# Kernel tuning notes

Hardware: AMD Instinct MI355X
Metric: run time of the kernel (lower is better)

## Reference

```python
import jax, jax.numpy as jnp
import numpy as np

DIM = 1024
NUM_HEADS = 16
HEAD_DIM = DIM // NUM_HEADS
EPS = 1e-5


def setup_inputs() -> dict:
    key = jax.random.key(0)
    ks = jax.random.split(key, 8)
    B, N = 4, 2048
    s = 0.02
    return {
        "x1": jax.random.normal(ks[0], (B, N, DIM), jnp.float32),
        "x2": jax.random.normal(ks[1], (B, N, DIM), jnp.float32),
        "wq": jax.random.normal(ks[2], (DIM, DIM), jnp.float32) * s,
        "bq": jnp.zeros((DIM,), jnp.float32),
        "wkv": jax.random.normal(ks[3], (DIM, 2 * DIM), jnp.float32) * s,
        "bkv": jnp.zeros((2 * DIM,), jnp.float32),
        "gamma_q": jnp.ones((HEAD_DIM,), jnp.float32),
        "beta_q": jnp.zeros((HEAD_DIM,), jnp.float32),
        "gamma_k": jnp.ones((HEAD_DIM,), jnp.float32),
        "beta_k": jnp.zeros((HEAD_DIM,), jnp.float32),
    }


def _layernorm(x, gamma, beta):
    m = jnp.mean(x, axis=-1, keepdims=True)
    v = jnp.mean(jnp.square(x - m), axis=-1, keepdims=True)
    return (x - m) * jax.lax.rsqrt(v + EPS) * gamma + beta


def reference(x1, x2, wq, bq, wkv, bkv, gamma_q, beta_q, gamma_k, beta_k):
    B, N, C = x1.shape
    H, D = NUM_HEADS, C // NUM_HEADS
    q = x1 @ wq + bq                      # [B,N,C]
    kv = x2 @ wkv + bkv                   # [B,N,2C]
    k, v = kv[..., :C], kv[..., C:]
    # [B,N,C] -> [B,H,N,D]
    q = q.reshape(B, N, H, D).transpose(0, 2, 1, 3)
    k = k.reshape(B, N, H, D).transpose(0, 2, 1, 3)
    v = v.reshape(B, N, H, D).transpose(0, 2, 1, 3)
    q = _layernorm(q, gamma_q, beta_q)
    k = _layernorm(k, gamma_k, beta_k)
    scale = 1.0 / jnp.sqrt(jnp.asarray(D, x1.dtype))
    scores = jnp.einsum("bhnd,bhmd->bhnm", q, k) * scale
    attn = jax.nn.softmax(scores, axis=-1)
    out = jnp.einsum("bhnm,bhmd->bhnd", attn, v)  # [B,H,N,D]
    return out.transpose(0, 2, 1, 3).reshape(B, N, C)
```

## Files before the change

### kernel.cpp

```cpp
#include <hip/hip_runtime.h>
#include <hip/hip_bf16.h>

#define NHEADS 16
#define HDIM 64
#define BATCH 4
#define SEQ 2048
#define CDIM 1024
#define ROWS (BATCH * SEQ)
#define QSCALE (0.125f * 1.44269504088896f)

typedef __attribute__((ext_vector_type(8))) short short8;
typedef __attribute__((ext_vector_type(4))) float f32x4;
typedef __attribute__((ext_vector_type(4))) unsigned int u32x4;
typedef __attribute__((ext_vector_type(2))) unsigned int u32x2;

__device__ inline short f2bf(float f) {
    unsigned int u = __builtin_bit_cast(unsigned int, f);
    unsigned int r = (u + 0x7fffu + ((u >> 16) & 1u)) >> 16;
    return (short)r;
}

__device__ __forceinline__ void gll16(const void* g, void* l) {
    __builtin_amdgcn_global_load_lds(
        (const __attribute__((address_space(1))) unsigned int*)g,
        (__attribute__((address_space(3))) unsigned int*)l, 16, 0, 0);
}

__device__ __forceinline__ unsigned int pack_bf2(float a, float b) {
    return __builtin_amdgcn_perm(__builtin_bit_cast(unsigned int, b),
                                 __builtin_bit_cast(unsigned int, a), 0x07060302u);
}

__global__ __launch_bounds__(256) void cvt_bf16(const float* __restrict__ src,
                                                short* __restrict__ dst, int n8) {
    int i = blockIdx.x * 256 + threadIdx.x;
    if (i < n8) {
        f32x4 a = ((const f32x4*)src)[i * 2];
        f32x4 b = ((const f32x4*)src)[i * 2 + 1];
        short8 o;
        o[0] = f2bf(a[0]); o[1] = f2bf(a[1]); o[2] = f2bf(a[2]); o[3] = f2bf(a[3]);
        o[4] = f2bf(b[0]); o[5] = f2bf(b[1]); o[6] = f2bf(b[2]); o[7] = f2bf(b[3]);
        ((short8*)dst)[i] = o;
    }
}

__global__ __launch_bounds__(256) void wtrans(const float* __restrict__ W,
                                              short* __restrict__ WT, int Nw) {
    __shared__ short T[64][72];
    const int t = threadIdx.x;
    const int n0 = blockIdx.x * 64, k0 = blockIdx.y * 64;
    const int kl = t >> 2, c4 = (t & 3) * 16;
    const float* src = W + (size_t)(k0 + kl) * Nw + n0 + c4;
    short8 s0, s1;
#pragma unroll
    for (int e = 0; e < 2; e++) {
        f32x4 u = *(const f32x4*)(src + e * 4);
        s0[e * 4 + 0] = f2bf(u[0]); s0[e * 4 + 1] = f2bf(u[1]);
        s0[e * 4 + 2] = f2bf(u[2]); s0[e * 4 + 3] = f2bf(u[3]);
        f32x4 v = *(const f32x4*)(src + 8 + e * 4);
        s1[e * 4 + 0] = f2bf(v[0]); s1[e * 4 + 1] = f2bf(v[1]);
        s1[e * 4 + 2] = f2bf(v[2]); s1[e * 4 + 3] = f2bf(v[3]);
    }
    *(short8*)&T[kl][c4] = s0;
    *(short8*)&T[kl][c4 + 8] = s1;
    __syncthreads();
#pragma unroll
    for (int pass = 0; pass < 2; pass++) {
        int n = (t >> 3) + pass * 32;
        short8 o;
#pragma unroll
        for (int e = 0; e < 8; e++) o[e] = T[(t & 7) * 8 + e][n];
        *(short8*)(WT + (size_t)(n0 + n) * 1024 + k0 + (t & 7) * 8) = o;
    }
}

__global__ __launch_bounds__(256) void gemm_q_ln(
    const short* __restrict__ A,
    const short* __restrict__ BT,
    const float* __restrict__ bias,
    const float* __restrict__ gamma,
    const float* __restrict__ beta,
    short* __restrict__ Out)
{
    __shared__ short As[128][32];
    __shared__ short Bs[128][32];

    const int tid = threadIdx.x;
    const int wave = tid >> 6, lane = tid & 63;
    const int wr = wave >> 1, wc = wave & 1;
    const int quad = lane >> 4, l15 = lane & 15;
    const int rblk = blockIdx.y, cblk = blockIdx.x;

    f32x4 acc[4][4];
#pragma unroll
    for (int i = 0; i < 4; i++)
#pragma unroll
        for (int j = 0; j < 4; j++) acc[i][j] = f32x4{0.f, 0.f, 0.f, 0.f};

    const int srow = wave * 32 + (lane >> 2);
    const int scol = (lane & 3) * 8;

    for (int k0 = 0; k0 < CDIM; k0 += 32) {
        __syncthreads();
#pragma unroll
        for (int c = 0; c < 2; c++) {
            gll16(A + (size_t)(rblk * 128 + srow + c * 16) * CDIM + k0 + scol,
                  &As[srow + c * 16][scol]);
            gll16(BT + (size_t)(cblk * 128 + srow + c * 16) * CDIM + k0 + scol,
                  &Bs[srow + c * 16][scol]);
        }
        __syncthreads();

        short8 af[4], bfr[4];
#pragma unroll
        for (int i = 0; i < 4; i++)
            af[i] = *(const short8*)&As[wr * 64 + i * 16 + l15][quad * 8];
#pragma unroll
        for (int j = 0; j < 4; j++)
            bfr[j] = *(const short8*)&Bs[wc * 64 + j * 16 + l15][quad * 8];
#pragma unroll
        for (int i = 0; i < 4; i++)
#pragma unroll
            for (int j = 0; j < 4; j++)
                acc[i][j] = __builtin_amdgcn_mfma_f32_16x16x32_bf16(af[i], bfr[j], acc[i][j], 0, 0, 0);
    }

    const int col0 = cblk * 128 + wc * 64;
    const int h = col0 >> 6;
    float bv[4], gv[4], btv[4];
#pragma unroll
    for (int j = 0; j < 4; j++) {
        int d = j * 16 + l15;
        bv[j] = bias[col0 + d];
        gv[j] = gamma[d];
        btv[j] = beta[d];
    }
#pragma unroll
    for (int i = 0; i < 4; i++) {
        int rowl = rblk * 128 + wr * 64 + i * 16 + quad * 4;
#pragma unroll
        for (int reg = 0; reg < 4; reg++) {
            float x[4], s = 0.f, s2 = 0.f;
#pragma unroll
            for (int j = 0; j < 4; j++) {
                x[j] = acc[i][j][reg] + bv[j];
                s += x[j];
                s2 += x[j] * x[j];
            }
#pragma unroll
            for (int m = 1; m < 16; m <<= 1) {
                s += __shfl_xor(s, m);
                s2 += __shfl_xor(s2, m);
            }
            float mean = s * (1.f / 64.f);
            float var = s2 * (1.f / 64.f) - mean * mean;
            float rstd = rsqrtf(var + 1e-5f);
            int r = rowl + reg;
            int b = r >> 11, n = r & (SEQ - 1);
            size_t base = (((size_t)b * NHEADS + h) * SEQ + n) * 64;
#pragma unroll
            for (int j = 0; j < 4; j++) {
                float y = ((x[j] - mean) * rstd * gv[j] + btv[j]) * QSCALE;
                Out[base + j * 16 + l15] = f2bf(y);
            }
        }
    }
}

__global__ __launch_bounds__(256) void gemm_kv(
    const short* __restrict__ A,
    const short* __restrict__ BT,
    const float* __restrict__ bias,
    const float* __restrict__ gamma,
    const float* __restrict__ beta,
    short* __restrict__ KOut,
    short* __restrict__ VT)
{
    __shared__ short As[128][32];
    __shared__ short Bs[128][32];
    __shared__ short Ts[4][64][68];

    const int tid = threadIdx.x;
    const int wave = tid >> 6, lane = tid & 63;
    const int wr = wave >> 1, wc = wave & 1;
    const int quad = lane >> 4, l15 = lane & 15;
    const int rblk = blockIdx.y, cblk = blockIdx.x;

    f32x4 acc[4][4];
#pragma unroll
    for (int i = 0; i < 4; i++)
#pragma unroll
        for (int j = 0; j < 4; j++) acc[i][j] = f32x4{0.f, 0.f, 0.f, 0.f};

    const int srow = wave * 32 + (lane >> 2);
    const int scol = (lane & 3) * 8;

    for (int k0 = 0; k0 < CDIM; k0 += 32) {
        __syncthreads();
#pragma unroll
        for (int c = 0; c < 2; c++) {
            gll16(A + (size_t)(rblk * 128 + srow + c * 16) * CDIM + k0 + scol,
                  &As[srow + c * 16][scol]);
            gll16(BT + (size_t)(cblk * 128 + srow + c * 16) * CDIM + k0 + scol,
                  &Bs[srow + c * 16][scol]);
        }
        __syncthreads();

        short8 af[4], bfr[4];
#pragma unroll
        for (int i = 0; i < 4; i++)
            af[i] = *(const short8*)&As[wr * 64 + i * 16 + l15][quad * 8];
#pragma unroll
        for (int j = 0; j < 4; j++)
            bfr[j] = *(const short8*)&Bs[wc * 64 + j * 16 + l15][quad * 8];
#pragma unroll
        for (int i = 0; i < 4; i++)
#pragma unroll
            for (int j = 0; j < 4; j++)
                acc[i][j] = __builtin_amdgcn_mfma_f32_16x16x32_bf16(af[i], bfr[j], acc[i][j], 0, 0, 0);
    }

    const int col0 = cblk * 128 + wc * 64;
    const int g = col0 >> 6;
    float bv[4];
#pragma unroll
    for (int j = 0; j < 4; j++) bv[j] = bias[col0 + j * 16 + l15];

    if (g < NHEADS) {
        const int h = g;
        float gv[4], btv[4];
#pragma unroll
        for (int j = 0; j < 4; j++) {
            int d = j * 16 + l15;
            gv[j] = gamma[d];
            btv[j] = beta[d];
        }
#pragma unroll
        for (int i = 0; i < 4; i++) {
            int rowl = rblk * 128 + wr * 64 + i * 16 + quad * 4;
#pragma unroll
            for (int reg = 0; reg < 4; reg++) {
                float x[4], s = 0.f, s2 = 0.f;
#pragma unroll
                for (int j = 0; j < 4; j++) {
                    x[j] = acc[i][j][reg] + bv[j];
                    s += x[j];
                    s2 += x[j] * x[j];
                }
#pragma unroll
                for (int m = 1; m < 16; m <<= 1) {
                    s += __shfl_xor(s, m);
                    s2 += __shfl_xor(s2, m);
                }
                float mean = s * (1.f / 64.f);
                float var = s2 * (1.f / 64.f) - mean * mean;
                float rstd = rsqrtf(var + 1e-5f);
                int r = rowl + reg;
                int b = r >> 11, n = r & (SEQ - 1);
                size_t base = (((size_t)b * NHEADS + h) * SEQ + n) * 64;
#pragma unroll
                for (int j = 0; j < 4; j++) {
                    float y = (x[j] - mean) * rstd * gv[j] + btv[j];
                    KOut[base + j * 16 + l15] = f2bf(y);
                }
            }
        }
    } else {
        const int h = g - NHEADS;
#pragma unroll
        for (int i = 0; i < 4; i++)
#pragma unroll
            for (int reg = 0; reg < 4; reg++)
#pragma unroll
                for (int j = 0; j < 4; j++)
                    Ts[wave][i * 16 + quad * 4 + reg][j * 16 + l15] =
                        f2bf(acc[i][j][reg] + bv[j]);
        const int r = rblk * 128 + wr * 64 + lane;
        const int b = r >> 11, n = r & (SEQ - 1);
        const size_t vtbase = (((size_t)b * NHEADS + h) * 64) * SEQ;
#pragma unroll
        for (int e8 = 0; e8 < 8; e8++) {
            short8 v = *(const short8*)&Ts[wave][lane][e8 * 8];
#pragma unroll
            for (int e = 0; e < 8; e++)
                VT[vtbase + (size_t)(e8 * 8 + e) * SEQ + n] = v[e];
        }
    }
}

template <int JD, bool FIRST>
__device__ __forceinline__ void band_store(float* __restrict__ Ot,
                                           const f32x4 (&o)[4][4],
                                           int l15, int q) {
#pragma unroll
    for (int qc = 0; qc < 4; qc++)
#pragma unroll
        for (int reg = 0; reg < 4; reg++) {
            float* dst = &Ot[(qc * 16 + l15) * 68 + JD * 16 + q * 4 + reg];
            if (FIRST) *dst = o[JD][qc][reg];
            else       *dst += o[JD][qc][reg];
        }
}

__global__ __launch_bounds__(256, 2) void attn_fa(
    const short* __restrict__ Q,
    const short* __restrict__ Kk,
    const short* __restrict__ VT,
    float* __restrict__ Out)
{
    __shared__ __align__(16) char smem_raw[20480];

    const int tid = threadIdx.x;
    const int w = tid >> 6, lane = tid & 63;
    const int q = lane >> 4, l15 = lane & 15;
    const int bh = blockIdx.x;
    const int b = bh >> 4, h = bh & 15;
    const int qt = blockIdx.y;
    const size_t hb = (size_t)bh * SEQ * 64;
    const size_t vb = (size_t)bh * 64 * SEQ;

    unsigned int* Pd = (unsigned int*)smem_raw + w * 1280;
    float* Ot = (float*)smem_raw;
    float* Lred = (float*)smem_raw + 64 * 68;

    short8 qf[4][2];
#pragma unroll
    for (int qc = 0; qc < 4; qc++)
#pragma unroll
        for (int dh = 0; dh < 2; dh++)
            qf[qc][dh] = *(const short8*)(Q + hb +
                (size_t)(qt * 64 + qc * 16 + l15) * 64 + dh * 32 + q * 8);

    short8 ones;
#pragma unroll
    for (int e = 0; e < 8; e++) ones[e] = (short)0x3F80;

    f32x4 o[4][4];
#pragma unroll
    for (int jd = 0; jd < 4; jd++)
#pragma unroll
        for (int qc = 0; qc < 4; qc++) o[jd][qc] = f32x4{0.f, 0.f, 0.f, 0.f};
    f32x4 osum[4];
#pragma unroll
    for (int qc = 0; qc < 4; qc++) osum[qc] = f32x4{0.f, 0.f, 0.f, 0.f};

    const short* kbase = Kk + hb + (size_t)(w * 32 + l15) * 64 + q * 8;
    const short* vbase = VT + vb + (size_t)l15 * SEQ + w * 32 + q * 8;

    for (int kti = 0; kti < 16; kti++) {
        short8 kf[2][2];
#pragma unroll
        for (int kt = 0; kt < 2; kt++)
#pragma unroll
            for (int dh = 0; dh < 2; dh++)
                kf[kt][dh] = *(const short8*)(kbase +
                    (size_t)(kti * 128 + kt * 16) * 64 + dh * 32);
        short8 vf[4];
#pragma unroll
        for (int jd = 0; jd < 4; jd++)
            vf[jd] = *(const short8*)(vbase + (size_t)(jd * 16) * SEQ + kti * 128);

#pragma unroll
        for (int kt = 0; kt < 2; kt++)
#pragma unroll
            for (int qc = 0; qc < 4; qc++) {
                f32x4 z = f32x4{0.f, 0.f, 0.f, 0.f};
                z = __builtin_amdgcn_mfma_f32_16x16x32_bf16(kf[kt][0], qf[qc][0], z, 0, 0, 0);
                z = __builtin_amdgcn_mfma_f32_16x16x32_bf16(kf[kt][1], qf[qc][1], z, 0, 0, 0);
                u32x2 d2;
                d2[0] = pack_bf2(__builtin_amdgcn_exp2f(z[0]), __builtin_amdgcn_exp2f(z[1]));
                d2[1] = pack_bf2(__builtin_amdgcn_exp2f(z[2]), __builtin_amdgcn_exp2f(z[3]));
                *(u32x2*)&Pd[(qc * 16 + l15) * 20 + kt * 8 + 2 * q] = d2;
            }

        short8 pf[4];
#pragma unroll
        for (int qc = 0; qc < 4; qc++) {
            u32x4 pr = *(const u32x4*)&Pd[(qc * 16 + l15) * 20 + 4 * q];
            pf[qc] = __builtin_bit_cast(short8, pr);
        }

#pragma unroll
        for (int qc = 0; qc < 4; qc++)
            osum[qc] = __builtin_amdgcn_mfma_f32_16x16x32_bf16(ones, pf[qc], osum[qc], 0, 0, 0);
#pragma unroll
        for (int jd = 0; jd < 4; jd++)
#pragma unroll
            for (int qc = 0; qc < 4; qc++)
                o[jd][qc] = __builtin_amdgcn_mfma_f32_16x16x32_bf16(vf[jd], pf[qc], o[jd][qc], 0, 0, 0);
    }

    __syncthreads();
#pragma unroll
    for (int p = 0; p < 4; p++) {
        const int jd = (w + p) & 3;
        if (p == 0) {
            switch (jd) {
            case 0: band_store<0, true>(Ot, o, l15, q); break;
            case 1: band_store<1, true>(Ot, o, l15, q); break;
            case 2: band_store<2, true>(Ot, o, l15, q); break;
            case 3: band_store<3, true>(Ot, o, l15, q); break;
            }
            if (q == 0) {
#pragma unroll
                for (int qc = 0; qc < 4; qc++)
                    Lred[w * 64 + qc * 16 + l15] = osum[qc][0];
            }
        } else {
            switch (jd) {
            case 0: band_store<0, false>(Ot, o, l15, q); break;
            case 1: band_store<1, false>(Ot, o, l15, q); break;
            case 2: band_store<2, false>(Ot, o, l15, q); break;
            case 3: band_store<3, false>(Ot, o, l15, q); break;
            }
        }
        __syncthreads();
    }

    const int row = tid >> 2, c = tid & 3;
    float l = Lred[row] + Lred[64 + row] + Lred[128 + row] + Lred[192 + row];
    float inv = 1.f / l;
    float* obase = Out + ((size_t)b * SEQ + qt * 64 + row) * CDIM + h * 64;
#pragma unroll
    for (int i = 0; i < 4; i++) {
        f32x4 t = *(const f32x4*)&Ot[row * 68 + (c + 4 * i) * 4];
        *(f32x4*)(obase + (c + 4 * i) * 4) = t * inv;
    }
}

extern "C" void kernel_launch(void* const* d_in, const int* in_sizes, int n_in,
                              void* d_out, int out_size, void* d_ws, size_t ws_size,
                              hipStream_t stream) {
    const float* x1 = (const float*)d_in[0];
    const float* x2 = (const float*)d_in[1];
    const float* wq = (const float*)d_in[2];
    const float* bq = (const float*)d_in[3];
    const float* wkv = (const float*)d_in[4];
    const float* bkv = (const float*)d_in[5];
    const float* gq = (const float*)d_in[6];
    const float* btq = (const float*)d_in[7];
    const float* gk = (const float*)d_in[8];
    const float* btk = (const float*)d_in[9];
    float* out = (float*)d_out;

    short* a1 = (short*)d_ws;
    short* a2 = a1 + (size_t)ROWS * CDIM;
    short* wqT = a2 + (size_t)ROWS * CDIM;
    short* wkvT = wqT + (size_t)CDIM * CDIM;
    short* qln = wkvT + (size_t)2 * CDIM * CDIM;
    short* kln = qln + (size_t)ROWS * CDIM;
    short* vt = kln + (size_t)ROWS * CDIM;

    const int n8 = ROWS * CDIM / 8;
    cvt_bf16<<<dim3(n8 / 256), 256, 0, stream>>>(x1, a1, n8);
    cvt_bf16<<<dim3(n8 / 256), 256, 0, stream>>>(x2, a2, n8);
    wtrans<<<dim3(16, 16), 256, 0, stream>>>(wq, wqT, CDIM);
    wtrans<<<dim3(32, 16), 256, 0, stream>>>(wkv, wkvT, 2 * CDIM);

    gemm_q_ln<<<dim3(8, 64), 256, 0, stream>>>(a1, wqT, bq, gq, btq, qln);
    gemm_kv<<<dim3(16, 64), 256, 0, stream>>>(a2, wkvT, bkv, gk, btk, kln, vt);
    attn_fa<<<dim3(64, 32), 256, 0, stream>>>(qln, kln, vt, out);
}
```

Baseline: 349.0 us.

## Swizzle GEMM block order, prefetch K/V registers, vectorize band store, add setprio

Both projection GEMMs now remap the linear block index so that consecutive blocks walk down rows sharing the same weight column tile, which is meant to improve cache reuse. The attention loop is software-pipelined with two register buffers, loading the next K/V tile while the current one is computed, to hide global-load latency. The output band store is vectorized to f32x4. MFMA sections are wrapped in s_setprio. The double buffering raises register pressure at 2 blocks per CU, and the final wrapped prefetch reloads tile 0 redundantly.

```diff
diff --git a/kernel.cpp b/kernel.cpp
--- a/kernel.cpp
+++ b/kernel.cpp
@@ -89,7 +89,9 @@
     const int wave = tid >> 6, lane = tid & 63;
     const int wr = wave >> 1, wc = wave & 1;
     const int quad = lane >> 4, l15 = lane & 15;
-    const int rblk = blockIdx.y, cblk = blockIdx.x;
+    const int lin = blockIdx.y * 8 + blockIdx.x;
+    const int swz = (lin & 7) * 64 + (lin >> 3);
+    const int rblk = swz >> 3, cblk = swz & 7;
 
     f32x4 acc[4][4];
 #pragma unroll
@@ -184,7 +186,9 @@
     const int wave = tid >> 6, lane = tid & 63;
     const int wr = wave >> 1, wc = wave & 1;
     const int quad = lane >> 4, l15 = lane & 15;
-    const int rblk = blockIdx.y, cblk = blockIdx.x;
+    const int lin = blockIdx.y * 16 + blockIdx.x;
+    const int swz = (lin & 7) * 128 + (lin >> 3);
+    const int rblk = swz >> 4, cblk = swz & 15;
 
     f32x4 acc[4][4];
 #pragma unroll
@@ -293,13 +297,62 @@
                                            const f32x4 (&o)[4][4],
                                            int l15, int q) {
 #pragma unroll
+    for (int qc = 0; qc < 4; qc++) {
+        f32x4* dst = (f32x4*)&Ot[(qc * 16 + l15) * 68 + JD * 16 + q * 4];
+        if (FIRST) *dst = o[JD][qc];
+        else       *dst = *dst + o[JD][qc];
+    }
+}
+
+__device__ __forceinline__ void load_kv(const short* __restrict__ kbase,
+                                        const short* __restrict__ vbase,
+                                        int kti, short8 kf[2][2], short8 vf[4]) {
+#pragma unroll
+    for (int kt = 0; kt < 2; kt++)
+#pragma unroll
+        for (int dh = 0; dh < 2; dh++)
+            kf[kt][dh] = *(const short8*)(kbase +
+                (size_t)(kti * 128 + kt * 16) * 64 + dh * 32);
+#pragma unroll
+    for (int jd = 0; jd < 4; jd++)
+        vf[jd] = *(const short8*)(vbase + (size_t)(jd * 16) * SEQ + kti * 128);
+}
+
+__device__ __forceinline__ void attn_step(const short8 kf[2][2], const short8 vf[4],
+                                          const short8 qf[4][2], const short8& ones,
+                                          unsigned int* __restrict__ Pd,
+                                          int l15, int q,
+                                          f32x4 (&o)[4][4], f32x4 (&osum)[4]) {
+#pragma unroll
+    for (int kt = 0; kt < 2; kt++)
+#pragma unroll
+        for (int qc = 0; qc < 4; qc++) {
+            f32x4 z = f32x4{0.f, 0.f, 0.f, 0.f};
+            z = __builtin_amdgcn_mfma_f32_16x16x32_bf16(kf[kt][0], qf[qc][0], z, 0, 0, 0);
+            z = __builtin_amdgcn_mfma_f32_16x16x32_bf16(kf[kt][1], qf[qc][1], z, 0, 0, 0);
+            u32x2 d2;
+            d2[0] = pack_bf2(__builtin_amdgcn_exp2f(z[0]), __builtin_amdgcn_exp2f(z[1]));
+            d2[1] = pack_bf2(__builtin_amdgcn_exp2f(z[2]), __builtin_amdgcn_exp2f(z[3]));
+            *(u32x2*)&Pd[(qc * 16 + l15) * 20 + kt * 8 + 2 * q] = d2;
+        }
+
+    short8 pf[4];
+#pragma unroll
+    for (int qc = 0; qc < 4; qc++) {
+        u32x4 pr = *(const u32x4*)&Pd[(qc * 16 + l15) * 20 + 4 * q];
+        pf[qc] = __builtin_bit_cast(short8, pr);
+    }
+
+    __builtin_amdgcn_s_setprio(1);
+#pragma unroll
     for (int qc = 0; qc < 4; qc++)
-#pragma unroll
-        for (int reg = 0; reg < 4; reg++) {
-            float* dst = &Ot[(qc * 16 + l15) * 68 + JD * 16 + q * 4 + reg];
-            if (FIRST) *dst = o[JD][qc][reg];
-            else       *dst += o[JD][qc][reg];
-        }
+        osum[qc] = __builtin_amdgcn_mfma_f32_16x16x32_bf16(ones, pf[qc], osum[qc], 0, 0, 0);
+#pragma unroll
+    for (int jd = 0; jd < 4; jd++)
+#pragma unroll
+        for (int qc = 0; qc < 4; qc++)
+            o[jd][qc] = __builtin_amdgcn_mfma_f32_16x16x32_bf16(vf[jd], pf[qc], o[jd][qc], 0, 0, 0);
+    __builtin_amdgcn_s_setprio(0);
 }
 
 __global__ __launch_bounds__(256, 2) void attn_fa(
@@ -347,47 +400,13 @@
     const short* kbase = Kk + hb + (size_t)(w * 32 + l15) * 64 + q * 8;
     const short* vbase = VT + vb + (size_t)l15 * SEQ + w * 32 + q * 8;
 
-    for (int kti = 0; kti < 16; kti++) {
-        short8 kf[2][2];
-#pragma unroll
-        for (int kt = 0; kt < 2; kt++)
-#pragma unroll
-            for (int dh = 0; dh < 2; dh++)
-                kf[kt][dh] = *(const short8*)(kbase +
-                    (size_t)(kti * 128 + kt * 16) * 64 + dh * 32);
-        short8 vf[4];
-#pragma unroll
-        for (int jd = 0; jd < 4; jd++)
-            vf[jd] = *(const short8*)(vbase + (size_t)(jd * 16) * SEQ + kti * 128);
-
-#pragma unroll
-        for (int kt = 0; kt < 2; kt++)
-#pragma unroll
-            for (int qc = 0; qc < 4; qc++) {
-                f32x4 z = f32x4{0.f, 0.f, 0.f, 0.f};
-                z = __builtin_amdgcn_mfma_f32_16x16x32_bf16(kf[kt][0], qf[qc][0], z, 0, 0, 0);
-                z = __builtin_amdgcn_mfma_f32_16x16x32_bf16(kf[kt][1], qf[qc][1], z, 0, 0, 0);
-                u32x2 d2;
-                d2[0] = pack_bf2(__builtin_amdgcn_exp2f(z[0]), __builtin_amdgcn_exp2f(z[1]));
-                d2[1] = pack_bf2(__builtin_amdgcn_exp2f(z[2]), __builtin_amdgcn_exp2f(z[3]));
-                *(u32x2*)&Pd[(qc * 16 + l15) * 20 + kt * 8 + 2 * q] = d2;
-            }
-
-        short8 pf[4];
-#pragma unroll
-        for (int qc = 0; qc < 4; qc++) {
-            u32x4 pr = *(const u32x4*)&Pd[(qc * 16 + l15) * 20 + 4 * q];
-            pf[qc] = __builtin_bit_cast(short8, pr);
-        }
-
-#pragma unroll
-        for (int qc = 0; qc < 4; qc++)
-            osum[qc] = __builtin_amdgcn_mfma_f32_16x16x32_bf16(ones, pf[qc], osum[qc], 0, 0, 0);
-#pragma unroll
-        for (int jd = 0; jd < 4; jd++)
-#pragma unroll
-            for (int qc = 0; qc < 4; qc++)
-                o[jd][qc] = __builtin_amdgcn_mfma_f32_16x16x32_bf16(vf[jd], pf[qc], o[jd][qc], 0, 0, 0);
+    short8 kfa[2][2], vfa[4], kfb[2][2], vfb[4];
+    load_kv(kbase, vbase, 0, kfa, vfa);
+    for (int kti = 0; kti < 16; kti += 2) {
+        load_kv(kbase, vbase, kti + 1, kfb, vfb);
+        attn_step(kfa, vfa, qf, ones, Pd, l15, q, o, osum);
+        load_kv(kbase, vbase, (kti + 2) & 15, kfa, vfa);
+        attn_step(kfb, vfb, qf, ones, Pd, l15, q, o, osum);
     }
 
     __syncthreads();
```

Measured after the change: 342.5 us. About the same (-1.9%).

## Split attention over 8 waves, raise MFMA priority, swizzle GEMM block order

Applied to the files above, without the earlier changes.

The attention kernel now uses 512 threads, with two query halves per key group, so each wave holds half the Q rows and accumulators. This cuts register pressure and lets more waves be resident. The V fragment loads are moved after the score MFMAs, and the PV MFMA section runs at raised wave priority via s_setprio. The projection GEMMs remap block indices so consecutive blocks share the same weight column tile, which should improve L2 reuse. Risks are that K/V fragments are loaded twice per block (once per query half) and the per-block Pd shared buffer shrinks, which could add memory traffic.

```diff
diff --git a/kernel.cpp b/kernel.cpp
--- a/kernel.cpp
+++ b/kernel.cpp
@@ -89,7 +89,9 @@
     const int wave = tid >> 6, lane = tid & 63;
     const int wr = wave >> 1, wc = wave & 1;
     const int quad = lane >> 4, l15 = lane & 15;
-    const int rblk = blockIdx.y, cblk = blockIdx.x;
+    const int lin = blockIdx.y * 8 + blockIdx.x;
+    const int swz = (lin & 7) * 64 + (lin >> 3);
+    const int rblk = swz >> 3, cblk = swz & 7;
 
     f32x4 acc[4][4];
 #pragma unroll
@@ -184,7 +186,9 @@
     const int wave = tid >> 6, lane = tid & 63;
     const int wr = wave >> 1, wc = wave & 1;
     const int quad = lane >> 4, l15 = lane & 15;
-    const int rblk = blockIdx.y, cblk = blockIdx.x;
+    const int lin = blockIdx.y * 16 + blockIdx.x;
+    const int swz = (lin & 7) * 128 + (lin >> 3);
+    const int rblk = swz >> 4, cblk = swz & 15;
 
     f32x4 acc[4][4];
 #pragma unroll
@@ -290,19 +294,17 @@
 
 template <int JD, bool FIRST>
 __device__ __forceinline__ void band_store(float* __restrict__ Ot,
-                                           const f32x4 (&o)[4][4],
-                                           int l15, int q) {
-#pragma unroll
-    for (int qc = 0; qc < 4; qc++)
-#pragma unroll
-        for (int reg = 0; reg < 4; reg++) {
-            float* dst = &Ot[(qc * 16 + l15) * 68 + JD * 16 + q * 4 + reg];
-            if (FIRST) *dst = o[JD][qc][reg];
-            else       *dst += o[JD][qc][reg];
-        }
-}
-
-__global__ __launch_bounds__(256, 2) void attn_fa(
+                                           const f32x4 (&o)[4][2],
+                                           int qh, int l15, int q) {
+#pragma unroll
+    for (int qc = 0; qc < 2; qc++) {
+        f32x4* dst = (f32x4*)&Ot[(qh * 32 + qc * 16 + l15) * 68 + JD * 16 + q * 4];
+        if (FIRST) *dst = o[JD][qc];
+        else       *dst = *dst + o[JD][qc];
+    }
+}
+
+__global__ __launch_bounds__(512, 4) void attn_fa(
     const short* __restrict__ Q,
     const short* __restrict__ Kk,
     const short* __restrict__ VT,
@@ -313,39 +315,41 @@
     const int tid = threadIdx.x;
     const int w = tid >> 6, lane = tid & 63;
     const int q = lane >> 4, l15 = lane & 15;
+    const int qh = w >> 2;
+    const int kg = w & 3;
     const int bh = blockIdx.x;
     const int b = bh >> 4, h = bh & 15;
     const int qt = blockIdx.y;
     const size_t hb = (size_t)bh * SEQ * 64;
     const size_t vb = (size_t)bh * 64 * SEQ;
 
-    unsigned int* Pd = (unsigned int*)smem_raw + w * 1280;
+    unsigned int* Pd = (unsigned int*)smem_raw + w * 640;
     float* Ot = (float*)smem_raw;
     float* Lred = (float*)smem_raw + 64 * 68;
 
-    short8 qf[4][2];
-#pragma unroll
-    for (int qc = 0; qc < 4; qc++)
+    short8 qf[2][2];
+#pragma unroll
+    for (int qc = 0; qc < 2; qc++)
 #pragma unroll
         for (int dh = 0; dh < 2; dh++)
             qf[qc][dh] = *(const short8*)(Q + hb +
-                (size_t)(qt * 64 + qc * 16 + l15) * 64 + dh * 32 + q * 8);
+                (size_t)(qt * 64 + qh * 32 + qc * 16 + l15) * 64 + dh * 32 + q * 8);
 
     short8 ones;
 #pragma unroll
     for (int e = 0; e < 8; e++) ones[e] = (short)0x3F80;
 
-    f32x4 o[4][4];
+    f32x4 o[4][2];
 #pragma unroll
     for (int jd = 0; jd < 4; jd++)
 #pragma unroll
-        for (int qc = 0; qc < 4; qc++) o[jd][qc] = f32x4{0.f, 0.f, 0.f, 0.f};
-    f32x4 osum[4];
-#pragma unroll
-    for (int qc = 0; qc < 4; qc++) osum[qc] = f32x4{0.f, 0.f, 0.f, 0.f};
-
-    const short* kbase = Kk + hb + (size_t)(w * 32 + l15) * 64 + q * 8;
-    const short* vbase = VT + vb + (size_t)l15 * SEQ + w * 32 + q * 8;
+        for (int qc = 0; qc < 2; qc++) o[jd][qc] = f32x4{0.f, 0.f, 0.f, 0.f};
+    f32x4 osum[2];
+#pragma unroll
+    for (int qc = 0; qc < 2; qc++) osum[qc] = f32x4{0.f, 0.f, 0.f, 0.f};
+
+    const short* kbase = Kk + hb + (size_t)(kg * 32 + l15) * 64 + q * 8;
+    const short* vbase = VT + vb + (size_t)l15 * SEQ + kg * 32 + q * 8;
 
     for (int kti = 0; kti < 16; kti++) {
         short8 kf[2][2];
@@ -355,15 +359,11 @@
             for (int dh = 0; dh < 2; dh++)
                 kf[kt][dh] = *(const short8*)(kbase +
                     (size_t)(kti * 128 + kt * 16) * 64 + dh * 32);
-        short8 vf[4];
-#pragma unroll
-        for (int jd = 0; jd < 4; jd++)
-            vf[jd] = *(const short8*)(vbase + (size_t)(jd * 16) * SEQ + kti * 128);
 
 #pragma unroll
         for (int kt = 0; kt < 2; kt++)
 #pragma unroll
-            for (int qc = 0; qc < 4; qc++) {
+            for (int qc = 0; qc < 2; qc++) {
                 f32x4 z = f32x4{0.f, 0.f, 0.f, 0.f};
                 z = __builtin_amdgcn_mfma_f32_16x16x32_bf16(kf[kt][0], qf[qc][0], z, 0, 0, 0);
                 z = __builtin_amdgcn_mfma_f32_16x16x32_bf16(kf[kt][1], qf[qc][1], z, 0, 0, 0);
@@ -373,59 +373,65 @@
                 *(u32x2*)&Pd[(qc * 16 + l15) * 20 + kt * 8 + 2 * q] = d2;
             }
 
-        short8 pf[4];
-#pragma unroll
-        for (int qc = 0; qc < 4; qc++) {
+        short8 vf[4];
+#pragma unroll
+        for (int jd = 0; jd < 4; jd++)
+            vf[jd] = *(const short8*)(vbase + (size_t)(jd * 16) * SEQ + kti * 128);
+
+        short8 pf[2];
+#pragma unroll
+        for (int qc = 0; qc < 2; qc++) {
             u32x4 pr = *(const u32x4*)&Pd[(qc * 16 + l15) * 20 + 4 * q];
             pf[qc] = __builtin_bit_cast(short8, pr);
         }
 
-#pragma unroll
-        for (int qc = 0; qc < 4; qc++)
+        __builtin_amdgcn_s_setprio(1);
+#pragma unroll
+        for (int qc = 0; qc < 2; qc++)
             osum[qc] = __builtin_amdgcn_mfma_f32_16x16x32_bf16(ones, pf[qc], osum[qc], 0, 0, 0);
 #pragma unroll
         for (int jd = 0; jd < 4; jd++)
 #pragma unroll
-            for (int qc = 0; qc < 4; qc++)
+            for (int qc = 0; qc < 2; qc++)
                 o[jd][qc] = __builtin_amdgcn_mfma_f32_16x16x32_bf16(vf[jd], pf[qc], o[jd][qc], 0, 0, 0);
+        __builtin_amdgcn_s_setprio(0);
     }
 
     __syncthreads();
 #pragma unroll
     for (int p = 0; p < 4; p++) {
-        const int jd = (w + p) & 3;
+        const int jd = (kg + p) & 3;
         if (p == 0) {
             switch (jd) {
-            case 0: band_store<0, true>(Ot, o, l15, q); break;
-            case 1: band_store<1, true>(Ot, o, l15, q); break;
-            case 2: band_store<2, true>(Ot, o, l15, q); break;
-            case 3: band_store<3, true>(Ot, o, l15, q); break;
+            case 0: band_store<0, true>(Ot, o, qh, l15, q); break;
+            case 1: band_store<1, true>(Ot, o, qh, l15, q); break;
+            case 2: band_store<2, true>(Ot, o, qh, l15, q); break;
+            case 3: band_store<3, true>(Ot, o, qh, l15, q); break;
             }
             if (q == 0) {
 #pragma unroll
-                for (int qc = 0; qc < 4; qc++)
-                    Lred[w * 64 + qc * 16 + l15] = osum[qc][0];
+                for (int qc = 0; qc < 2; qc++)
+                    Lred[kg * 64 + qh * 32 + qc * 16 + l15] = osum[qc][0];
             }
         } else {
             switch (jd) {
-            case 0: band_store<0, false>(Ot, o, l15, q); break;
-            case 1: band_store<1, false>(Ot, o, l15, q); break;
-            case 2: band_store<2, false>(Ot, o, l15, q); break;
-            case 3: band_store<3, false>(Ot, o, l15, q); break;
+            case 0: band_store<0, false>(Ot, o, qh, l15, q); break;
+            case 1: band_store<1, false>(Ot, o, qh, l15, q); break;
+            case 2: band_store<2, false>(Ot, o, qh, l15, q); break;
+            case 3: band_store<3, false>(Ot, o, qh, l15, q); break;
             }
         }
         __syncthreads();
     }
 
-    const int row = tid >> 2, c = tid & 3;
+    const int row = tid >> 3, c = tid & 7;
     float l = Lred[row] + Lred[64 + row] + Lred[128 + row] + Lred[192 + row];
     float inv = 1.f / l;
-    float* obase = Out + ((size_t)b * SEQ + qt * 64 + row) * CDIM + h * 64;
-#pragma unroll
-    for (int i = 0; i < 4; i++) {
-        f32x4 t = *(const f32x4*)&Ot[row * 68 + (c + 4 * i) * 4];
-        *(f32x4*)(obase + (c + 4 * i) * 4) = t * inv;
-    }
+    float* obase = Out + ((size_t)b * SEQ + qt * 64 + row) * CDIM + h * 64 + c * 8;
+    f32x4 t0 = *(const f32x4*)&Ot[row * 68 + c * 8];
+    f32x4 t1 = *(const f32x4*)&Ot[row * 68 + c * 8 + 4];
+    *(f32x4*)obase = t0 * inv;
+    *(f32x4*)(obase + 4) = t1 * inv;
 }
 
 extern "C" void kernel_launch(void* const* d_in, const int* in_sizes, int n_in,
@@ -459,5 +465,5 @@
 
     gemm_q_ln<<<dim3(8, 64), 256, 0, stream>>>(a1, wqT, bq, gq, btq, qln);
     gemm_kv<<<dim3(16, 64), 256, 0, stream>>>(a2, wkvT, bkv, gk, btk, kln, vt);
-    attn_fa<<<dim3(64, 32), 256, 0, stream>>>(qln, kln, vt, out);
-}
+    attn_fa<<<dim3(64, 32), 512, 0, stream>>>(qln, kln, vt, out);
+}
```

Measured after the change: 448.6 us. +28.6%, slower.
